# Kernel tuning notes

Hardware: AMD Instinct MI355X
Metric: run time of the kernel (lower is better)

Reference implementation:

```python
import jax, jax.numpy as jnp
import numpy as np

N_STROKE = 100000
N_BREP = 50000
E = 1600000
D_IN, D_H = 6, 32
# (src_type, dst_type, aggregation) for the 5 hard-coded relations, in order:
# intersects_mean, temp_previous_add, represented_by_mean, brepcoplanar_max, strokecoplanar_max
RELS = [("stroke", "stroke", "mean"),
        ("stroke", "stroke", "add"),
        ("stroke", "brep", "mean"),
        ("brep", "brep", "max"),
        ("stroke", "stroke", "max")]

def _nnodes(nt):
    return N_STROKE if nt == "stroke" else N_BREP

def _aggregate(x_src, src, dst, n_dst, aggr):
    msg = x_src[src]  # [E, d] gather
    if aggr == "add":
        return jax.ops.segment_sum(msg, dst, num_segments=n_dst)
    if aggr == "mean":
        s = jax.ops.segment_sum(msg, dst, num_segments=n_dst)
        cnt = jax.ops.segment_sum(jnp.ones((msg.shape[0],), msg.dtype), dst, num_segments=n_dst)
        return s / jnp.maximum(cnt, 1.0)[:, None]
    # max: empty segments come back -inf -> replace with 0 like PyG
    m = jax.ops.segment_max(msg, dst, num_segments=n_dst)
    return jnp.where(jnp.isfinite(m), m, jnp.zeros_like(m))

def hetero_conv(x, eis, W_rel, b_rel, W_root):
    # GraphConv per relation: lin_rel(aggr(x_src)) + lin_root(x_dst); HeteroConv aggr='sum'
    d_out = W_rel.shape[2]
    out = {"stroke": jnp.zeros((N_STROKE, d_out), x["stroke"].dtype),
           "brep": jnp.zeros((N_BREP, d_out), x["brep"].dtype)}
    for i, (st, dt, aggr) in enumerate(RELS):
        src, dst = eis[i][0], eis[i][1]
        agg = _aggregate(x[st], src, dst, _nnodes(dt), aggr)
        out[dt] = out[dt] + agg @ W_rel[i] + b_rel[i] + x[dt] @ W_root[i]
    return out

def setup_inputs() -> dict:
    key = jax.random.key(0)
    ks = jax.random.split(key, 16)
    def ei(k, ns, nd):
        return jnp.stack([jax.random.randint(k, (E,), 0, ns, dtype=jnp.int64) if False else jax.random.randint(k, (E,), 0, ns).astype(jnp.int64),
                          jax.random.randint(jax.random.fold_in(k, 1), (E,), 0, nd).astype(jnp.int64)])
    inp = {
        "x_stroke": jax.random.normal(ks[0], (N_STROKE, D_IN), jnp.float32),
        "x_brep": jax.random.normal(ks[1], (N_BREP, D_IN), jnp.float32),
        "ei_intersects": ei(ks[2], N_STROKE, N_STROKE),
        "ei_temp_previous": ei(ks[3], N_STROKE, N_STROKE),
        "ei_represented_by": ei(ks[4], N_STROKE, N_BREP),
        "ei_brepcoplanar": ei(ks[5], N_BREP, N_BREP),
        "ei_strokecoplanar": ei(ks[6], N_STROKE, N_STROKE),
        # local_head params: per-relation lin_rel and lin_root, 6 -> 32
        "W0_rel": 0.1 * jax.random.normal(ks[7], (5, D_IN, D_H), jnp.float32),
        "b0_rel": jnp.zeros((5, D_H), jnp.float32),
        "W0_root": 0.1 * jax.random.normal(ks[8], (5, D_IN, D_H), jnp.float32),
        # 4 residual blocks, per-relation, 32 -> 32
        "Wb_rel": 0.1 * jax.random.normal(ks[9], (4, 5, D_H, D_H), jnp.float32),
        "bb_rel": jnp.zeros((4, 5, D_H), jnp.float32),
        "Wb_root": 0.1 * jax.random.normal(ks[10], (4, 5, D_H, D_H), jnp.float32),
    }
    return inp

def reference(x_stroke, x_brep, ei_intersects, ei_temp_previous, ei_represented_by,
              ei_brepcoplanar, ei_strokecoplanar, W0_rel, b0_rel, W0_root,
              Wb_rel, bb_rel, Wb_root):
    eis = [ei_intersects, ei_temp_previous, ei_represented_by, ei_brepcoplanar, ei_strokecoplanar]
    x = {"stroke": x_stroke, "brep": x_brep}
    x = hetero_conv(x, eis, W0_rel, b0_rel, W0_root)
    for l in range(4):  # 4 residual hetero-conv blocks
        h = hetero_conv(x, eis, Wb_rel[l], bb_rel[l], Wb_root[l])
        x = {k: x[k] + h[k] for k in x}
    return (jax.nn.relu(x["stroke"]), jax.nn.relu(x["brep"]))
```

## Files before the change

### kernel.cpp

```cpp
#include <hip/hip_runtime.h>
#include <math.h>

#define NS 100000
#define NB 50000
#define EE 1600000

#define BSH 8
#define BSZ 256
#define NBK_S ((NS + BSZ - 1) / BSZ)
#define NBK_B ((NB + BSZ - 1) / BSZ)
#define CHUNK 16384
#define NCH ((EE + CHUNK - 1) / CHUNK)

#define SRC_MASK 0x1FFFF
#define SSH 17

typedef unsigned int u32;
typedef unsigned short u16;


__global__ __launch_bounds__(256) void hist_kernel(
    const int* __restrict__ e0, const int* __restrict__ e1, const int* __restrict__ e2,
    const int* __restrict__ e3, const int* __restrict__ e4, int* __restrict__ bcnt)
{
    int j = blockIdx.x, rel = blockIdx.y, tid = threadIdx.x;
    const int* ei = (rel == 0) ? e0 : (rel == 1) ? e1 : (rel == 2) ? e2 : (rel == 3) ? e3 : e4;
    int nb = (rel == 2 || rel == 3) ? NBK_B : NBK_S;
    __shared__ int hist[NBK_S];
    for (int i = tid; i < nb; i += 256) hist[i] = 0;
    __syncthreads();
    int es = j * CHUNK, ee2 = min(EE, es + CHUNK);
    for (int e = es + tid; e < ee2; e += 256)
        atomicAdd(&hist[ei[EE + e] >> BSH], 1);
    __syncthreads();
    for (int i = tid; i < nb; i += 256)
        if (hist[i]) atomicAdd(&bcnt[rel * NBK_S + i], hist[i]);
}


__global__ __launch_bounds__(512) void bscan_kernel(const int* __restrict__ bcnt,
                                                    int* __restrict__ bbase,
                                                    int* __restrict__ gcur)
{
    int rel = blockIdx.x;
    int nb = (rel == 2 || rel == 3) ? NBK_B : NBK_S;
    __shared__ int s[512];
    int tid = threadIdx.x;
    int v = (tid < nb) ? bcnt[rel * NBK_S + tid] : 0;
    s[tid] = v;
    __syncthreads();
    for (int off = 1; off < 512; off <<= 1) {
        int t = (tid >= off) ? s[tid - off] : 0;
        __syncthreads();
        s[tid] += t;
        __syncthreads();
    }
    int ex = s[tid] - v;
    if (tid < nb) { bbase[rel * NBK_S + tid] = ex; gcur[rel * NBK_S + tid] = ex; }
}


__global__ __launch_bounds__(256, 2) void sort_kernel(
    const int* __restrict__ e0, const int* __restrict__ e1, const int* __restrict__ e2,
    const int* __restrict__ e3, const int* __restrict__ e4,
    int* __restrict__ ebkt, int* __restrict__ gcur)
{
    int j = blockIdx.x, rel = blockIdx.y, tid = threadIdx.x;
    const int* ei = (rel == 0) ? e0 : (rel == 1) ? e1 : (rel == 2) ? e2 : (rel == 3) ? e3 : e4;
    int nb = (rel == 2 || rel == 3) ? NBK_B : NBK_S;

    __shared__ int start[NBK_S + 1];
    __shared__ int cur[NBK_S];
    __shared__ int gbase[NBK_S];
    __shared__ int part[256];
    __shared__ int buf[CHUNK];

    int es = j * CHUNK, ee2 = min(EE, es + CHUNK);
    int n = ee2 - es;

    for (int i = tid; i < nb; i += 256) cur[i] = 0;
    __syncthreads();
    for (int e = es + tid; e < ee2; e += 256)
        atomicAdd(&cur[ei[EE + e] >> BSH], 1);
    __syncthreads();

    int v0 = (2 * tid < nb) ? cur[2 * tid] : 0;
    int v1 = (2 * tid + 1 < nb) ? cur[2 * tid + 1] : 0;
    part[tid] = v0 + v1;
    __syncthreads();
    for (int off = 1; off < 256; off <<= 1) {
        int t = (tid >= off) ? part[tid - off] : 0;
        __syncthreads();
        part[tid] += t;
        __syncthreads();
    }
    int run = (tid > 0) ? part[tid - 1] : 0;
    if (2 * tid < nb) start[2 * tid] = run;
    if (2 * tid + 1 < nb) start[2 * tid + 1] = run + v0;
    if (tid == 0) start[nb] = n;
    __syncthreads();
    for (int i = tid; i < nb; i += 256) cur[i] = start[i];
    __syncthreads();

    for (int e = es + tid; e < ee2; e += 256) {
        int s = ei[e], d = ei[EE + e];
        int pos = atomicAdd(&cur[d >> BSH], 1);
        buf[pos] = ((d & (BSZ - 1)) << SSH) | s;
    }
    for (int b = tid; b < nb; b += 256) {
        int c = start[b + 1] - start[b];
        gbase[b] = c ? atomicAdd(&gcur[rel * NBK_S + b], c) : 0;
    }
    __syncthreads();

    int* eo = ebkt + (size_t)rel * EE;
    for (int i = tid; i < n; i += 256) {
        int lo = 0, hi = nb;
        while (hi - lo > 1) { int mid = (lo + hi) >> 1; if (start[mid] <= i) lo = mid; else hi = mid; }
        eo[gbase[lo] + (i - start[lo])] = buf[i];
    }
}


__global__ __launch_bounds__(256, 8) void csr_kernel(
    const int* __restrict__ ebkt, const int* __restrict__ bcnt, const int* __restrict__ bbase,
    int* __restrict__ edges_csr, int* __restrict__ rs_all)
{
    int bkt = blockIdx.x, rel = blockIdx.y, tid = threadIdx.x;
    int nb = (rel == 2 || rel == 3) ? NBK_B : NBK_S;
    if (bkt >= nb) return;
    int nd = (rel == 2 || rel == 3) ? NB : NS;

    int base = bbase[rel * NBK_S + bkt];
    int cnt = bcnt[rel * NBK_S + bkt];
    const int* span = ebkt + (size_t)rel * EE + base;
    int* rs = rs_all + rel * (NS + 1);

    __shared__ int h[BSZ], s[BSZ], cu[BSZ];
    h[tid] = 0;
    __syncthreads();
    for (int i = tid; i < cnt; i += 256)
        atomicAdd(&h[span[i] >> SSH], 1);
    __syncthreads();
    s[tid] = h[tid];
    __syncthreads();
    for (int off = 1; off < 256; off <<= 1) {
        int t = (tid >= off) ? s[tid - off] : 0;
        __syncthreads();
        s[tid] += t;
        __syncthreads();
    }
    int exv = s[tid] - h[tid];
    cu[tid] = exv;
    int node = bkt * BSZ + tid;
    if (node < nd) rs[node] = base + exv;
    if (bkt == nb - 1 && tid == 0) rs[nd] = base + cnt;
    __syncthreads();

    int* outp = edges_csr + (size_t)rel * EE;
    for (int i = tid; i < cnt; i += 256) {
        int p = span[i];
        int pos = atomicAdd(&cu[p >> SSH], 1);
        outp[base + pos] = p & SRC_MASK;
    }
}


__device__ __forceinline__ u32 bfpack(float a, float b) {
    u32 ua = __float_as_uint(a), ub = __float_as_uint(b);
    ua = (ua + 0x7fffu + ((ua >> 16) & 1u)) >> 16;
    ub = (ub + 0x7fffu + ((ub >> 16) & 1u)) >> 16;
    return ua | (ub << 16);
}
__device__ __forceinline__ u16 bf1(float f) {
    u32 u = __float_as_uint(f);
    return (u16)((u + 0x7fffu + ((u >> 16) & 1u)) >> 16);
}
__device__ __forceinline__ float bflo(u32 u) { return __uint_as_float(u << 16); }
__device__ __forceinline__ float bfhi(u32 u) { return __uint_as_float(u & 0xffff0000u); }


template <int AGGR>
__device__ __forceinline__ float4 gath32bf(const u32* __restrict__ xsrc,
                                           const int* __restrict__ srcs,
                                           int s0, int deg, int md, int li, int l8)
{
    float init = (AGGR == 2) ? -INFINITY : 0.f;
    float4 acc = {init, init, init, init};
    for (int bs = 0; bs < md; bs += 8) {
        int a = s0 + bs + l8;
        int idx = srcs[a < (EE - 1) ? a : (EE - 1)];
        #pragma unroll
        for (int jj = 0; jj < 8; ++jj) {
            int s = __shfl(idx, (li & ~7) + jj, 64);
            if (bs + jj < deg) {
                uint2 v = *reinterpret_cast<const uint2*>(xsrc + (size_t)s * 16 + l8 * 2);
                float f0 = bflo(v.x), f1 = bfhi(v.x), f2 = bflo(v.y), f3 = bfhi(v.y);
                if (AGGR == 2) {
                    acc.x = fmaxf(acc.x, f0); acc.y = fmaxf(acc.y, f1);
                    acc.z = fmaxf(acc.z, f2); acc.w = fmaxf(acc.w, f3);
                } else {
                    acc.x += f0; acc.y += f1; acc.z += f2; acc.w += f3;
                }
            }
        }
    }
    return acc;
}

template <int AGGR>
__device__ __forceinline__ float gath6(const float* __restrict__ xsrc,
                                       const int* __restrict__ srcs,
                                       int s0, int deg, int md, int li, int l8)
{
    float acc = (AGGR == 2) ? -INFINITY : 0.f;
    for (int bs = 0; bs < md; bs += 8) {
        int a = s0 + bs + l8;
        int idx = srcs[a < (EE - 1) ? a : (EE - 1)];
        #pragma unroll
        for (int jj = 0; jj < 8; ++jj) {
            int s = __shfl(idx, (li & ~7) + jj, 64);
            if (bs + jj < deg && l8 < 6) {
                float v = xsrc[(size_t)s * 6 + l8];
                if (AGGR == 2) acc = fmaxf(acc, v); else acc += v;
            }
        }
    }
    return acc;
}


struct FRel {
    const int* rs;
    const int* srcs;
    const void* xsrc;
    const float* W;
    const float* b;
    const float* Wroot;
};

template <int D, int AGGR>
__device__ __forceinline__ void do_gather(const FRel& R, int node, int nd,
                                          int li, int l8, int nl,
                                          u32* aggP, float* aggF)
{
    int nodec = min(node, nd - 1);
    int s0 = R.rs[nodec];
    int deg = R.rs[nodec + 1] - s0;
    if (node >= nd) deg = 0;
    int md = deg;
    md = max(md, __shfl_xor(md, 8, 64));
    md = max(md, __shfl_xor(md, 16, 64));
    md = max(md, __shfl_xor(md, 32, 64));
    if (D == 32) {
        float4 acc = gath32bf<AGGR>((const u32*)R.xsrc, R.srcs, s0, deg, md, li, l8);
        if (AGGR == 1) { float inv = 1.f / (float)max(deg, 1); acc.x *= inv; acc.y *= inv; acc.z *= inv; acc.w *= inv; }
        if (AGGR == 2 && deg == 0) { acc.x = acc.y = acc.z = acc.w = 0.f; }
        aggP[nl * 16 + l8 * 2]     = bfpack(acc.x, acc.y);
        aggP[nl * 16 + l8 * 2 + 1] = bfpack(acc.z, acc.w);
    } else {
        float acc = gath6<AGGR>((const float*)R.xsrc, R.srcs, s0, deg, md, li, l8);
        if (AGGR == 1) acc *= 1.f / (float)max(deg, 1);
        if (AGGR == 2 && deg == 0) acc = 0.f;
        aggF[nl * 8 + l8] = (l8 < 6) ? acc : 0.f;
    }
}

template <int D, int NREL, bool RES, bool RELU, bool OUTBF, int A0, int A1, int A2>
__global__ __launch_bounds__(256, 8) void fused_kernel(
    FRel r0, FRel r1, FRel r2,
    const void* xdst, void* outp, int nd)
{
    __shared__ u32 sWb[(D == 32) ? NREL * 16 * 32 : 1];
    __shared__ float sW6[(D == 32) ? 1 : NREL * 6 * 32];
    __shared__ float sWr[D * 32];
    __shared__ u32 aggP[(D == 32) ? NREL * 32 * 16 : 1];
    __shared__ float aggF[(D == 32) ? 1 : NREL * 32 * 8];
    __shared__ u32 xP[(D == 32) ? 32 * 16 : 1];
    __shared__ float xF[(D == 32) ? 1 : 32 * 8];

    int tid = threadIdx.x, li = tid & 63, l8 = tid & 7, nl = tid >> 3;
    int node = blockIdx.x * 32 + nl;
    bool valid = node < nd;

    if (D == 32) {
        for (int i = tid; i < 16 * 32; i += 256) {
            int k2 = i >> 5, dim = i & 31;
            sWb[0 * 512 + i] = bfpack(r0.W[(2 * k2) * 32 + dim], r0.W[(2 * k2 + 1) * 32 + dim]);
            if (NREL > 1) sWb[1 * 512 + i] = bfpack(r1.W[(2 * k2) * 32 + dim], r1.W[(2 * k2 + 1) * 32 + dim]);
            if (NREL > 2) sWb[2 * 512 + i] = bfpack(r2.W[(2 * k2) * 32 + dim], r2.W[(2 * k2 + 1) * 32 + dim]);
        }
    } else {
        for (int i = tid; i < 6 * 32; i += 256) {
            sW6[0 * 192 + i] = r0.W[i];
            if (NREL > 1) sW6[1 * 192 + i] = r1.W[i];
            if (NREL > 2) sW6[2 * 192 + i] = r2.W[i];
        }
    }
    for (int i = tid; i < D * 32; i += 256) {
        float wv = r0.Wroot[i];
        if (NREL > 1) wv += r1.Wroot[i];
        if (NREL > 2) wv += r2.Wroot[i];
        sWr[i] = wv;
    }

    if (D == 32) {
        uint2 xv = {0u, 0u};
        if (valid) xv = *reinterpret_cast<const uint2*>((const u32*)xdst + (size_t)node * 16 + l8 * 2);
        xP[nl * 16 + l8 * 2] = xv.x;
        xP[nl * 16 + l8 * 2 + 1] = xv.y;
    } else {
        float xv = (valid && l8 < 6) ? ((const float*)xdst)[(size_t)node * 6 + l8] : 0.f;
        xF[nl * 8 + l8] = xv;
    }

    do_gather<D, A0>(r0, node, nd, li, l8, nl, aggP + 0 * 32 * 16, aggF + 0 * 32 * 8);
    if (NREL > 1) do_gather<D, A1>(r1, node, nd, li, l8, nl, aggP + 1 * 32 * 16, aggF + 1 * 32 * 8);
    if (NREL > 2) do_gather<D, A2>(r2, node, nd, li, l8, nl, aggP + 2 * 32 * 16, aggF + 2 * 32 * 8);

    __syncthreads();

    int dim = tid & 31, grp = tid >> 5;
    #pragma unroll
    for (int it = 0; it < 4; ++it) {
        int n2 = grp + it * 8;
        int gnode = blockIdx.x * 32 + n2;
        if (gnode < nd) {
            float mm = r0.b[dim];
            if (NREL > 1) mm += r1.b[dim];
            if (NREL > 2) mm += r2.b[dim];
            if (D == 32) {
                #pragma unroll
                for (int r = 0; r < NREL; ++r) {
                    const u32* ar = aggP + r * 32 * 16 + n2 * 16;
                    const u32* wr = sWb + r * 512;
                    #pragma unroll
                    for (int k2 = 0; k2 < 16; ++k2) {
                        u32 a = ar[k2];
                        u32 w = wr[k2 * 32 + dim];
                        mm = fmaf(bflo(a), bflo(w), mm);
                        mm = fmaf(bfhi(a), bfhi(w), mm);
                    }
                }
                const u32* xr = xP + n2 * 16;
                #pragma unroll
                for (int k2 = 0; k2 < 16; ++k2) {
                    u32 u = xr[k2];
                    mm = fmaf(bflo(u), sWr[(2 * k2) * 32 + dim], mm);
                    mm = fmaf(bfhi(u), sWr[(2 * k2 + 1) * 32 + dim], mm);
                }
                if (RES) {
                    u32 u = xr[dim >> 1];
                    mm += (dim & 1) ? bfhi(u) : bflo(u);
                }
            } else {
                #pragma unroll
                for (int r = 0; r < NREL; ++r)
                    #pragma unroll
                    for (int k = 0; k < 6; ++k)
                        mm = fmaf(aggF[r * 32 * 8 + n2 * 8 + k], sW6[r * 192 + k * 32 + dim], mm);
                #pragma unroll
                for (int k = 0; k < 6; ++k)
                    mm = fmaf(xF[n2 * 8 + k], sWr[k * 32 + dim], mm);
            }
            if (RELU) mm = fmaxf(mm, 0.f);
            if (OUTBF) ((u16*)outp)[(size_t)gnode * 32 + dim] = bf1(mm);
            else       ((float*)outp)[(size_t)gnode * 32 + dim] = mm;
        }
    }
}


static inline char* alignp(char* p, size_t a) {
    return (char*)(((uintptr_t)p + a - 1) & ~(a - 1));
}

extern "C" void kernel_launch(void* const* d_in, const int* in_sizes, int n_in,
                              void* d_out, int out_size, void* d_ws, size_t ws_size,
                              hipStream_t stream)
{
    const float* x_stroke = (const float*)d_in[0];
    const float* x_brep   = (const float*)d_in[1];
    const int* ei0 = (const int*)d_in[2];
    const int* ei1 = (const int*)d_in[3];
    const int* ei2 = (const int*)d_in[4];
    const int* ei3 = (const int*)d_in[5];
    const int* ei4 = (const int*)d_in[6];
    const float* W0_rel  = (const float*)d_in[7];
    const float* b0_rel  = (const float*)d_in[8];
    const float* W0_root = (const float*)d_in[9];
    const float* Wb_rel  = (const float*)d_in[10];
    const float* bb_rel  = (const float*)d_in[11];
    const float* Wb_root = (const float*)d_in[12];
    float* out = (float*)d_out;

    char* A = alignp((char*)d_ws, 256);
    int* ebkt = (int*)A;
    u32* xs0 = (u32*)A;
    u32* xb0 = xs0 + (size_t)NS * 16;
    char* Aend = (char*)(ebkt + (size_t)5 * EE);
    u32* xs1 = (u32*)alignp(Aend, 256);
    u32* xb1 = xs1 + (size_t)NS * 16;
    int* edges_csr = (int*)alignp((char*)(xb1 + (size_t)NB * 16), 256);
    int* rs_all = (int*)alignp((char*)(edges_csr + (size_t)5 * EE), 256);
    int* bcnt  = (int*)alignp((char*)(rs_all + 5 * (NS + 1)), 256);
    int* bbase = (int*)alignp((char*)(bcnt + 5 * NBK_S), 256);
    int* gcur  = (int*)alignp((char*)(bbase + 5 * NBK_S), 256);

    hipMemsetAsync(bcnt, 0, 5 * NBK_S * sizeof(int), stream);
    hist_kernel<<<dim3(NCH, 5), 256, 0, stream>>>(ei0, ei1, ei2, ei3, ei4, bcnt);
    bscan_kernel<<<5, 512, 0, stream>>>(bcnt, bbase, gcur);
    sort_kernel<<<dim3(NCH, 5), 256, 0, stream>>>(ei0, ei1, ei2, ei3, ei4, ebkt, gcur);
    csr_kernel<<<dim3(NBK_S, 5), 256, 0, stream>>>(ebkt, bcnt, bbase, edges_csr, rs_all);

    auto relW = [&](int l, int r) -> const float* {
        return l == 0 ? W0_rel + r * 6 * 32 : Wb_rel + ((l - 1) * 5 + r) * 32 * 32;
    };
    auto relB = [&](int l, int r) -> const float* {
        return l == 0 ? b0_rel + r * 32 : bb_rel + ((l - 1) * 5 + r) * 32;
    };
    auto relWr = [&](int l, int r) -> const float* {
        return l == 0 ? W0_root + r * 6 * 32 : Wb_root + ((l - 1) * 5 + r) * 32 * 32;
    };
    auto FR = [&](int l, int r, const void* xsrc) -> FRel {
        FRel R;
        R.rs = rs_all + r * (NS + 1);
        R.srcs = edges_csr + (size_t)r * EE;
        R.xsrc = xsrc;
        R.W = relW(l, r); R.b = relB(l, r); R.Wroot = relWr(l, r);
        return R;
    };

    const int GS = (NS + 31) / 32;
    const int GB = (NB + 31) / 32;

    fused_kernel<6, 3, false, false, true, 1, 0, 2><<<GS, 256, 0, stream>>>(
        FR(0, 0, x_stroke), FR(0, 1, x_stroke), FR(0, 4, x_stroke), x_stroke, xs0, NS);
    fused_kernel<6, 2, false, false, true, 1, 2, 0><<<GB, 256, 0, stream>>>(
        FR(0, 2, x_stroke), FR(0, 3, x_brep), FR(0, 2, x_stroke), x_brep, xb0, NB);

    const u32* cs = xs0; const u32* cb = xb0;
    for (int l = 1; l <= 3; ++l) {
        u32* os = (l & 1) ? xs1 : xs0;
        u32* ob = (l & 1) ? xb1 : xb0;
        fused_kernel<32, 3, true, false, true, 1, 0, 2><<<GS, 256, 0, stream>>>(
            FR(l, 0, cs), FR(l, 1, cs), FR(l, 4, cs), cs, os, NS);
        fused_kernel<32, 2, true, false, true, 1, 2, 0><<<GB, 256, 0, stream>>>(
            FR(l, 2, cs), FR(l, 3, cb), FR(l, 2, cs), cb, ob, NB);
        cs = os; cb = ob;
    }
    fused_kernel<32, 3, true, true, false, 1, 0, 2><<<GS, 256, 0, stream>>>(
        FR(4, 0, cs), FR(4, 1, cs), FR(4, 4, cs), cs, out, NS);
    fused_kernel<32, 2, true, true, false, 1, 2, 0><<<GB, 256, 0, stream>>>(
        FR(4, 2, cs), FR(4, 3, cb), FR(4, 2, cs), cb, out + (size_t)NS * 32, NB);

    (void)in_sizes; (void)n_in; (void)out_size; (void)ws_size;
}
```

Baseline: 843.1 us.

## Shrink sort chunks, write buckets per-wave, widen gather loads to 16B

The sort kernel now processes 8192-edge chunks with a smaller shared buffer so more blocks fit per CU. Its scatter phase walks buckets one wave at a time instead of binary-searching the bucket for every element. The 32-wide bf16 gather now has each lane load 16 bytes, with two half-groups of lanes taking alternate edges and combining through a cross-lane shuffle. Each node's loop now runs to its own degree rather than the max degree in the wave. This trades fewer, wider memory requests for extra shuffles and more loop divergence between lanes.

Result: faster. 711.6 us (-15.6%).

```diff
diff --git a/kernel.cpp b/kernel.cpp
--- a/kernel.cpp
+++ b/kernel.cpp
@@ -11,6 +11,8 @@
 #define NBK_B ((NB + BSZ - 1) / BSZ)
 #define CHUNK 16384
 #define NCH ((EE + CHUNK - 1) / CHUNK)
+#define SCH 8192
+#define NSC ((EE + SCH - 1) / SCH)
 
 #define SRC_MASK 0x1FFFF
 #define SSH 17
@@ -60,7 +62,7 @@
 }
 
 
-__global__ __launch_bounds__(256, 2) void sort_kernel(
+__global__ __launch_bounds__(256, 4) void sort_kernel(
     const int* __restrict__ e0, const int* __restrict__ e1, const int* __restrict__ e2,
     const int* __restrict__ e3, const int* __restrict__ e4,
     int* __restrict__ ebkt, int* __restrict__ gcur)
@@ -73,9 +75,9 @@
     __shared__ int cur[NBK_S];
     __shared__ int gbase[NBK_S];
     __shared__ int part[256];
-    __shared__ int buf[CHUNK];
-
-    int es = j * CHUNK, ee2 = min(EE, es + CHUNK);
+    __shared__ int buf[SCH];
+
+    int es = j * SCH, ee2 = min(EE, es + SCH);
     int n = ee2 - es;
 
     for (int i = tid; i < nb; i += 256) cur[i] = 0;
@@ -114,10 +116,11 @@
     __syncthreads();
 
     int* eo = ebkt + (size_t)rel * EE;
-    for (int i = tid; i < n; i += 256) {
-        int lo = 0, hi = nb;
-        while (hi - lo > 1) { int mid = (lo + hi) >> 1; if (start[mid] <= i) lo = mid; else hi = mid; }
-        eo[gbase[lo] + (i - start[lo])] = buf[i];
+    int w = tid >> 6, l = tid & 63;
+    for (int b = w; b < nb; b += 4) {
+        int sb = start[b], c = start[b + 1] - sb, gb = gbase[b];
+        for (int i = l; i < c; i += 64)
+            eo[gb + i] = buf[sb + i];
     }
 }
 
@@ -181,31 +184,48 @@
 
 
 template <int AGGR>
-__device__ __forceinline__ float4 gath32bf(const u32* __restrict__ xsrc,
-                                           const int* __restrict__ srcs,
-                                           int s0, int deg, int md, int li, int l8)
+__device__ __forceinline__ void gath32bf(const u32* __restrict__ xsrc,
+                                         const int* __restrict__ srcs,
+                                         int s0, int deg, int li, int l8,
+                                         float (&acc)[8])
 {
     float init = (AGGR == 2) ? -INFINITY : 0.f;
-    float4 acc = {init, init, init, init};
-    for (int bs = 0; bs < md; bs += 8) {
-        int a = s0 + bs + l8;
-        int idx = srcs[a < (EE - 1) ? a : (EE - 1)];
+    #pragma unroll
+    for (int d = 0; d < 8; ++d) acc[d] = init;
+    int grp = l8 >> 2, q = l8 & 3;
+    int lim = s0 + deg - 1;
+    int obase = li & ~7;
+    for (int bs = 0; bs < deg; bs += 16) {
+        int a0 = s0 + bs + 2 * l8;
+        int ix0 = srcs[a0 < lim ? a0 : lim];
+        int ix1 = srcs[a0 + 1 < lim ? a0 + 1 : lim];
         #pragma unroll
-        for (int jj = 0; jj < 8; ++jj) {
-            int s = __shfl(idx, (li & ~7) + jj, 64);
-            if (bs + jj < deg) {
-                uint2 v = *reinterpret_cast<const uint2*>(xsrc + (size_t)s * 16 + l8 * 2);
+        for (int sub = 0; sub < 8; ++sub) {
+            int sa = __shfl(ix0, obase + sub, 64);
+            int sb = __shfl(ix1, obase + sub, 64);
+            int s = grp ? sb : sa;
+            int e = bs + 2 * sub + grp;
+            if (e < deg) {
+                uint4 v = *reinterpret_cast<const uint4*>(xsrc + (size_t)s * 16 + q * 4);
                 float f0 = bflo(v.x), f1 = bfhi(v.x), f2 = bflo(v.y), f3 = bfhi(v.y);
+                float f4 = bflo(v.z), f5 = bfhi(v.z), f6 = bflo(v.w), f7 = bfhi(v.w);
                 if (AGGR == 2) {
-                    acc.x = fmaxf(acc.x, f0); acc.y = fmaxf(acc.y, f1);
-                    acc.z = fmaxf(acc.z, f2); acc.w = fmaxf(acc.w, f3);
+                    acc[0] = fmaxf(acc[0], f0); acc[1] = fmaxf(acc[1], f1);
+                    acc[2] = fmaxf(acc[2], f2); acc[3] = fmaxf(acc[3], f3);
+                    acc[4] = fmaxf(acc[4], f4); acc[5] = fmaxf(acc[5], f5);
+                    acc[6] = fmaxf(acc[6], f6); acc[7] = fmaxf(acc[7], f7);
                 } else {
-                    acc.x += f0; acc.y += f1; acc.z += f2; acc.w += f3;
+                    acc[0] += f0; acc[1] += f1; acc[2] += f2; acc[3] += f3;
+                    acc[4] += f4; acc[5] += f5; acc[6] += f6; acc[7] += f7;
                 }
             }
         }
     }
-    return acc;
+    #pragma unroll
+    for (int d = 0; d < 8; ++d) {
+        float o = __shfl_xor(acc[d], 4, 64);
+        acc[d] = (AGGR == 2) ? fmaxf(acc[d], o) : (acc[d] + o);
+    }
 }
 
 template <int AGGR>
@@ -248,17 +268,28 @@
     int s0 = R.rs[nodec];
     int deg = R.rs[nodec + 1] - s0;
     if (node >= nd) deg = 0;
-    int md = deg;
-    md = max(md, __shfl_xor(md, 8, 64));
-    md = max(md, __shfl_xor(md, 16, 64));
-    md = max(md, __shfl_xor(md, 32, 64));
     if (D == 32) {
-        float4 acc = gath32bf<AGGR>((const u32*)R.xsrc, R.srcs, s0, deg, md, li, l8);
-        if (AGGR == 1) { float inv = 1.f / (float)max(deg, 1); acc.x *= inv; acc.y *= inv; acc.z *= inv; acc.w *= inv; }
-        if (AGGR == 2 && deg == 0) { acc.x = acc.y = acc.z = acc.w = 0.f; }
-        aggP[nl * 16 + l8 * 2]     = bfpack(acc.x, acc.y);
-        aggP[nl * 16 + l8 * 2 + 1] = bfpack(acc.z, acc.w);
+        float acc[8];
+        gath32bf<AGGR>((const u32*)R.xsrc, R.srcs, s0, deg, li, l8, acc);
+        if (AGGR == 1) {
+            float inv = 1.f / (float)max(deg, 1);
+            #pragma unroll
+            for (int d = 0; d < 8; ++d) acc[d] *= inv;
+        }
+        if (AGGR == 2 && deg == 0) {
+            #pragma unroll
+            for (int d = 0; d < 8; ++d) acc[d] = 0.f;
+        }
+        int grp = l8 >> 2, q = l8 & 3;
+        uint2 o;
+        if (grp == 0) { o.x = bfpack(acc[0], acc[1]); o.y = bfpack(acc[2], acc[3]); }
+        else          { o.x = bfpack(acc[4], acc[5]); o.y = bfpack(acc[6], acc[7]); }
+        *reinterpret_cast<uint2*>(aggP + nl * 16 + q * 4 + grp * 2) = o;
     } else {
+        int md = deg;
+        md = max(md, __shfl_xor(md, 8, 64));
+        md = max(md, __shfl_xor(md, 16, 64));
+        md = max(md, __shfl_xor(md, 32, 64));
         float acc = gath6<AGGR>((const float*)R.xsrc, R.srcs, s0, deg, md, li, l8);
         if (AGGR == 1) acc *= 1.f / (float)max(deg, 1);
         if (AGGR == 2 && deg == 0) acc = 0.f;
@@ -410,7 +441,7 @@
     hipMemsetAsync(bcnt, 0, 5 * NBK_S * sizeof(int), stream);
     hist_kernel<<<dim3(NCH, 5), 256, 0, stream>>>(ei0, ei1, ei2, ei3, ei4, bcnt);
     bscan_kernel<<<5, 512, 0, stream>>>(bcnt, bbase, gcur);
-    sort_kernel<<<dim3(NCH, 5), 256, 0, stream>>>(ei0, ei1, ei2, ei3, ei4, ebkt, gcur);
+    sort_kernel<<<dim3(NSC, 5), 256, 0, stream>>>(ei0, ei1, ei2, ei3, ei4, ebkt, gcur);
     csr_kernel<<<dim3(NBK_S, 5), 256, 0, stream>>>(ebkt, bcnt, bbase, edges_csr, rs_all);
 
     auto relW = [&](int l, int r) -> const float* {
```
